# Performance work log

Hardware: AMD Instinct MI355X
Metric: run time of the kernel (lower is better)

Reference implementation:

```python
import jax, jax.numpy as jnp
import numpy as np

B, L, V, D, H, DEPTH, M, FF, NC = 16, 1000, 8, 512, 8, 6, 256, 2048, 1
DH = D // H
SCALE = DH ** -0.5
KCONV = 33  # residual depthwise conv kernel (lucidrains default)


def layer_norm(x, s, b):
    mu = x.mean(-1, keepdims=True)
    var = ((x - mu) ** 2).mean(-1, keepdims=True)
    return (x - mu) * jax.lax.rsqrt(var + 1e-5) * s + b


def moore_penrose_pinv(x, iters=6):
    # iterative Moore-Penrose pseudoinverse (Nystromformer paper / lucidrains)
    I = jnp.eye(x.shape[-1], dtype=x.dtype)
    ax = jnp.abs(x)
    z = jnp.swapaxes(x, -1, -2) / (jnp.max(ax.sum(-1)) * jnp.max(ax.sum(-2)))
    for _ in range(iters):
        xz = x @ z
        z = 0.25 * z @ (13 * I - xz @ (15 * I - xz @ (7 * I - xz)))
    return z


def nystrom_attention(x, qkv_w, out_w, out_b, conv_k):
    b, n, d = x.shape
    pad = (M - n % M) % M  # pad on the LEFT so seq divisible by num_landmarks
    xp = jnp.pad(x, ((0, 0), (pad, 0), (0, 0)))
    N = n + pad
    q, k, v = jnp.split(xp @ qkv_w, 3, axis=-1)
    rh = lambda t: t.reshape(b, N, H, DH).transpose(0, 2, 1, 3)  # bhnd
    q, k, v = rh(q) * SCALE, rh(k), rh(v)
    l = N // M
    q_l = q.reshape(b, H, M, l, DH).mean(3)  # landmark means
    k_l = k.reshape(b, H, M, l, DH).mean(3)
    attn1 = jax.nn.softmax(jnp.einsum('bhnd,bhmd->bhnm', q, k_l), -1)
    attn2 = jax.nn.softmax(jnp.einsum('bhnd,bhmd->bhnm', q_l, k_l), -1)
    attn3 = jax.nn.softmax(jnp.einsum('bhmd,bhnd->bhmn', q_l, k), -1)
    out = (attn1 @ moore_penrose_pinv(attn2)) @ (attn3 @ v)
    # residual depthwise conv over sequence, groups=heads (Conv2d(h,h,(33,1)))
    res = jax.lax.conv_general_dilated(
        v, conv_k, (1, 1), ((KCONV // 2, KCONV // 2), (0, 0)),
        feature_group_count=H, dimension_numbers=('NCHW', 'OIHW', 'NCHW'))
    out = (out + res).transpose(0, 2, 1, 3).reshape(b, N, d)
    out = out @ out_w + out_b
    return out[:, -n:]


def setup_inputs() -> dict:
    key = jax.random.key(0)
    ks = jax.random.split(key, 9)
    s = lambda k, shape, scale=0.02: jax.random.normal(k, shape, jnp.float32) * scale
    return {
        'x': jax.random.randint(ks[0], (B, L), 0, V),
        'enc_emb': s(ks[1], (V, D), 1.0),
        'pos_emb': s(ks[2], (L, D), 1.0),
        'ln1_s': jnp.ones((DEPTH, D)), 'ln1_b': jnp.zeros((DEPTH, D)),
        'qkv_w': s(ks[3], (DEPTH, D, 3 * D)),
        'attn_out_w': s(ks[4], (DEPTH, D, D)), 'attn_out_b': jnp.zeros((DEPTH, D)),
        'conv_k': s(ks[5], (DEPTH, H, 1, KCONV, 1)),
        'ln2_s': jnp.ones((DEPTH, D)), 'ln2_b': jnp.zeros((DEPTH, D)),
        'ff_w1': s(ks[6], (DEPTH, D, FF)), 'ff_b1': jnp.zeros((DEPTH, FF)),
        'ff_w2': s(ks[7], (DEPTH, FF, D)), 'ff_b2': jnp.zeros((DEPTH, D)),
        'final_w': s(ks[8], (D * L, NC)), 'final_b': jnp.zeros((NC,)),
    }


def reference(x, enc_emb, pos_emb, ln1_s, ln1_b, qkv_w, attn_out_w, attn_out_b,
              conv_k, ln2_s, ln2_b, ff_w1, ff_b1, ff_w2, ff_b2, final_w, final_b):
    h = enc_emb[x] + pos_emb[None, :, :]  # token emb + learned posenc
    for i in range(DEPTH):
        h = h + nystrom_attention(layer_norm(h, ln1_s[i], ln1_b[i]),
                                  qkv_w[i], attn_out_w[i], attn_out_b[i], conv_k[i])
        z = layer_norm(h, ln2_s[i], ln2_b[i])
        h = h + jax.nn.gelu(z @ ff_w1[i] + ff_b1[i], approximate=False) @ ff_w2[i] + ff_b2[i]
    out = h.reshape(B, -1) @ final_w + final_b
    return out.reshape(-1)
```

## Files before the change

kernel.cpp:

```cpp
#include <hip/hip_runtime.h>
#include <hip/hip_bf16.h>
#include <math.h>

typedef unsigned short u16;
typedef unsigned int   u32;
typedef __attribute__((ext_vector_type(8))) short short8;
typedef __attribute__((ext_vector_type(4))) float f32x4;

#define L_ 1000
#define D_ 512
#define N_ 1024
#define DEPTH_ 6
#define PAD_ 24
#define SCALE_ 0.125f

__device__ inline float bf2f(u16 u){ union{u32 i; float f;} x; x.i = ((u32)u) << 16; return x.f; }
__device__ inline u16 f2bf(float f){
  union{float f; u32 i;} x; x.f = f;
  u32 r = x.i + 0x7fffu + ((x.i >> 16) & 1u);
  return (u16)(r >> 16);
}

__device__ inline void gld16(const u16* g, u16* l){
  __builtin_amdgcn_global_load_lds(
      (const __attribute__((address_space(1))) unsigned*)g,
      (__attribute__((address_space(3))) unsigned*)l, 16, 0, 0);
}

__device__ inline float blockSum256(float v, float* red){
  int t = threadIdx.x;
  #pragma unroll
  for (int o = 32; o > 0; o >>= 1) v += __shfl_down(v, o, 64);
  __syncthreads();
  if ((t & 63) == 0) red[t >> 6] = v;
  __syncthreads();
  return red[0] + red[1] + red[2] + red[3];
}
__device__ inline float blockMax256(float v, float* red){
  int t = threadIdx.x;
  #pragma unroll
  for (int o = 32; o > 0; o >>= 1) v = fmaxf(v, __shfl_down(v, o, 64));
  __syncthreads();
  if ((t & 63) == 0) red[t >> 6] = v;
  __syncthreads();
  return fmaxf(fmaxf(red[0], red[1]), fmaxf(red[2], red[3]));
}

__global__ __launch_bounds__(256) void embed_kernel(
    const int* __restrict__ x, const float* __restrict__ ee,
    const float* __restrict__ pe, float* __restrict__ h)
{
  long long i = (long long)blockIdx.x * 256 + threadIdx.x;
  int d = (int)(i & 511);
  long long bl = i >> 9;
  int l = (int)(bl % 1000);
  int tok = x[bl];
  h[i] = ee[tok * D_ + d] + pe[l * D_ + d];
}

__global__ __launch_bounds__(256) void ln_kernel(
    const float* __restrict__ in, u16* __restrict__ out,
    const float* __restrict__ sc, const float* __restrict__ bi, int pad)
{
  __shared__ float red[4];
  int r = blockIdx.x, t = threadIdx.x;
  const float* row; u16* orow;
  if (pad){
    int bb = r >> 10, n = r & 1023;
    orow = out + (long long)r * D_;
    if (n < PAD_){ orow[t] = 0; orow[t + 256] = 0; return; }
    row = in + ((long long)bb * L_ + (n - PAD_)) * D_;
  } else {
    row  = in  + (long long)r * D_;
    orow = out + (long long)r * D_;
  }
  float x0 = row[t], x1 = row[t + 256];
  float mu = blockSum256(x0 + x1, red) * (1.f / 512.f);
  float d0 = x0 - mu, d1 = x1 - mu;
  float var = blockSum256(d0 * d0 + d1 * d1, red) * (1.f / 512.f);
  float rs = rsqrtf(var + 1e-5f);
  orow[t]       = f2bf(d0 * rs * sc[t]       + bi[t]);
  orow[t + 256] = f2bf(d1 * rs * sc[t + 256] + bi[t + 256]);
}

__global__ __launch_bounds__(256) void tconv_kernel(
    const float* __restrict__ src, u16* __restrict__ dst, int K, int N)
{
  __shared__ float tile[32][33];
  int kg = blockIdx.y << 5, ng = blockIdx.x << 5;
  int t = threadIdx.x;
  int kr = t >> 3, nc = (t & 7) << 2;
  float4 v = *(const float4*)(src + (long long)(kg + kr) * N + ng + nc);
  tile[kr][nc + 0] = v.x; tile[kr][nc + 1] = v.y;
  tile[kr][nc + 2] = v.z; tile[kr][nc + 3] = v.w;
  __syncthreads();
  int nr = t >> 3, kc = (t & 7) << 2;
  ushort4 o;
  o.x = f2bf(tile[kc + 0][nr]); o.y = f2bf(tile[kc + 1][nr]);
  o.z = f2bf(tile[kc + 2][nr]); o.w = f2bf(tile[kc + 3][nr]);
  *(ushort4*)(dst + (long long)(ng + nr) * K + kg + kc) = o;
}

__global__ __launch_bounds__(256) void vtrans_kernel(
    const u16* __restrict__ qkv, u16* __restrict__ vT)
{
  __shared__ u16 tile[32][36];
  int idx = blockIdx.x;
  int bh = idx >> 6, rem = idx & 63;
  int dt = rem >> 5, nt = rem & 31;
  int b = bh >> 3, hh = bh & 7;
  int t = threadIdx.x;
  {
    int nr = t >> 3, dc = (t & 7) << 2;
    const u16* src = qkv + ((long long)b * N_ + nt * 32 + nr) * 1536 + 1024 + hh * 64 + dt * 32 + dc;
    ushort4 v = *(const ushort4*)src;
    tile[nr][dc + 0] = v.x; tile[nr][dc + 1] = v.y;
    tile[nr][dc + 2] = v.z; tile[nr][dc + 3] = v.w;
  }
  __syncthreads();
  {
    int dr = t >> 3, nc = (t & 7) << 2;
    ushort4 o;
    o.x = tile[nc + 0][dr]; o.y = tile[nc + 1][dr];
    o.z = tile[nc + 2][dr]; o.w = tile[nc + 3][dr];
    *(ushort4*)(vT + (long long)bh * 65536 + (dt * 32 + dr) * 1024 + nt * 32 + nc) = o;
  }
}

template<int OUT, int WC, int TR>
__global__ __launch_bounds__(256) void mgemm(
    const u16* __restrict__ A16, const u16* __restrict__ B16, void* __restrict__ Cv,
    u16* __restrict__ CT, const float* __restrict__ bias,
    int M, int N, int K, int lda, int ldb, int ldc, int ldct,
    long long sAb, long long sAh, long long sBb, long long sBh,
    long long sCb, long long sCh, long long sCT, int nh,
    float scale, float alpha, float beta, int flags)
{
  __shared__ __align__(16) u16 SH[18432];
  u16* As = SH;
  u16* Bs = SH + 8192;

  const int t = threadIdx.x;
  const int bz = blockIdx.z;
  const int b = bz / nh, hh = bz - b * nh;
  const int m0 = blockIdx.y << 7, n0 = blockIdx.x << 7;

  const u16* A = A16 + (long long)b * sAb + (long long)hh * sAh;
  const u16* B = B16 + (long long)b * sBb + (long long)hh * sBh;

  f32x4 acc[4][4];
  #pragma unroll
  for (int i = 0; i < 4; i++)
    #pragma unroll
    for (int j = 0; j < 4; j++) acc[i][j] = (f32x4)0.f;

  const int w = t >> 6, lane = t & 63;
  const int wm = (w >> 1) << 6, wn = (w & 1) << 6;
  const int fr = lane & 15, ko = (lane >> 4) << 3;
  const int sw = (fr & 7) << 3;

  const int sr8 = lane >> 3;
  const int sc8 = ((lane & 7) ^ sr8) << 3;
  const u16* pa[4]; const u16* pb[4]; u16* la[4]; u16* lb[4];
  #pragma unroll
  for (int q = 0; q < 4; q++){
    int ra = min(m0 + w * 32 + q * 8 + sr8, M - 1);
    int rb = min(n0 + w * 32 + q * 8 + sr8, N - 1);
    pa[q] = A + (long long)ra * lda + sc8;
    pb[q] = B + (long long)rb * ldb + sc8;
    la[q] = As + (w * 32 + q * 8) * 64 + lane * 8;
    lb[q] = Bs + (w * 32 + q * 8) * 64 + lane * 8;
  }

  for (int k0 = 0; k0 < K; k0 += 64){
    #pragma unroll
    for (int q = 0; q < 4; q++) gld16(pa[q] + k0, la[q]);
    #pragma unroll
    for (int q = 0; q < 4; q++) gld16(pb[q] + k0, lb[q]);
    __syncthreads();

    #pragma unroll
    for (int ks = 0; ks < 2; ks++){
      short8 ah[4], bhh[4];
      #pragma unroll
      for (int i = 0; i < 4; i++)
        ah[i]  = *(const short8*)(As + (wm + i*16 + fr) * 64 + (((ks << 5) + ko) ^ sw));
      #pragma unroll
      for (int j = 0; j < 4; j++)
        bhh[j] = *(const short8*)(Bs + (wn + j*16 + fr) * 64 + (((ks << 5) + ko) ^ sw));
      #pragma unroll
      for (int i = 0; i < 4; i++)
        #pragma unroll
        for (int j = 0; j < 4; j++)
          acc[i][j] = __builtin_amdgcn_mfma_f32_16x16x32_bf16(ah[i], bhh[j], acc[i][j], 0, 0, 0);
    }
    __syncthreads();
  }

  const long long coff = (long long)b * sCb + (long long)hh * sCh;
  const int quad = (lane >> 4) << 2;
  #pragma unroll
  for (int i = 0; i < 4; i++){
    #pragma unroll
    for (int j = 0; j < 4; j++){
      #pragma unroll
      for (int r = 0; r < 4; r++){
        int row = m0 + wm + i*16 + quad + r;
        int col = n0 + wn + j*16 + fr;
        if (row < M && col < N){
          float v = acc[i][j][r];
          float at = (alpha != 0.f) ? bf2f(A[(long long)row * lda + col]) : 0.f;
          float bt = (beta  != 0.f) ? bf2f(B[(long long)col * ldb + row]) : 0.f;
          v = scale * (alpha * at + beta * bt - v);
          if (flags & 4) v -= (row == col) ? 1.f : 0.f;
          if (bias) v += bias[col];
          if (flags & 2) v = 0.5f * v * (1.f + erff(v * 0.7071067811865476f));
          if constexpr (WC){
            if constexpr (OUT == 0){
              float* cp = (float*)Cv + coff + (long long)row * ldc + col;
              if (flags & 1) v += *cp;
              *cp = v;
            } else {
              u16* cp = (u16*)Cv + coff + (long long)row * ldc + col;
              if (flags & 1) v += bf2f(*cp);
              *cp = f2bf(v);
            }
          }
          if constexpr (TR)
            SH[(wn + j*16 + fr) * 144 + (wm + i*16 + quad + r)] = f2bf(v);
        }
      }
    }
  }
  if constexpr (TR){
    __syncthreads();
    const long long cofft = (long long)bz * sCT;
    #pragma unroll
    for (int c2 = 0; c2 < 8; c2++){
      int idx = c2 * 256 + t;
      int cl = idx >> 4, ms = (idx & 15) << 3;
      int gcol = n0 + cl;
      if (gcol < N && m0 + ms < M){
        uint4 val = *(const uint4*)(SH + cl * 144 + ms);
        *(uint4*)(CT + cofft + (long long)gcol * ldct + m0 + ms) = val;
      }
    }
  }
}

__global__ __launch_bounds__(256) void fattn1_kernel(
    const u16* __restrict__ qkv, const u16* __restrict__ klp,
    const u16* __restrict__ wlT, u16* __restrict__ apre)
{
  __shared__ __align__(16) u16 LDS[20480];
  u16* Qs = LDS;
  u16* Ks = LDS + 4096;
  u16* Ps = LDS;
  const int t = threadIdx.x, w = t >> 6, lane = t & 63;
  const int bh = blockIdx.y, b = bh >> 3, hh = bh & 7;
  const int m0 = blockIdx.x << 6;
  const int fr = lane & 15, ko = (lane >> 4) << 3, sw = (fr & 7) << 3;
  const u16* wl = wlT + (long long)bh * 16384;

  {
    int sr = lane >> 3, sc = ((lane & 7) ^ sr) << 3;
    const u16* qbase = qkv + ((long long)b * N_ + m0) * 1536 + hh * 64 + sc;
    const u16* kbase = klp + (long long)bh * 16384 + sc;
    #pragma unroll
    for (int q = 0; q < 2; q++)
      gld16(qbase + (long long)(w*16 + q*8 + sr) * 1536, Qs + (w*16 + q*8) * 64 + lane * 8);
    #pragma unroll
    for (int q = 0; q < 8; q++)
      gld16(kbase + (w*64 + q*8 + sr) * 64, Ks + (w*64 + q*8) * 64 + lane * 8);
  }
  __syncthreads();

  f32x4 s[16];
  #pragma unroll
  for (int j = 0; j < 16; j++) s[j] = (f32x4)0.f;
  #pragma unroll
  for (int ks = 0; ks < 2; ks++){
    short8 aq = *(const short8*)(Qs + (w*16 + fr) * 64 + (((ks << 5) + ko) ^ sw));
    #pragma unroll
    for (int j = 0; j < 16; j++){
      short8 bk = *(const short8*)(Ks + (j*16 + fr) * 64 + (((ks << 5) + ko) ^ sw));
      s[j] = __builtin_amdgcn_mfma_f32_16x16x32_bf16(aq, bk, s[j], 0, 0, 0);
    }
  }
  __syncthreads();

  const int g4 = (lane >> 4) << 2, c = lane & 15;
  #pragma unroll
  for (int r = 0; r < 4; r++){
    float v[16]; float mx = -3.4e38f;
    #pragma unroll
    for (int j = 0; j < 16; j++){ v[j] = s[j][r] * SCALE_; mx = fmaxf(mx, v[j]); }
    #pragma unroll
    for (int m = 1; m < 16; m <<= 1) mx = fmaxf(mx, __shfl_xor(mx, m, 64));
    float sum = 0.f;
    #pragma unroll
    for (int j = 0; j < 16; j++){ v[j] = expf(v[j] - mx); sum += v[j]; }
    #pragma unroll
    for (int m = 1; m < 16; m <<= 1) sum += __shfl_xor(sum, m, 64);
    float inv = 1.f / sum;
    int row = w*16 + g4 + r;
    #pragma unroll
    for (int j = 0; j < 16; j++) Ps[row * 264 + j*16 + c] = f2bf(v[j] * inv);
  }

  f32x4 o[4];
  #pragma unroll
  for (int j = 0; j < 4; j++) o[j] = (f32x4)0.f;
  #pragma unroll
  for (int ks = 0; ks < 8; ks++){
    short8 ap = *(const short8*)(Ps + (w*16 + fr) * 264 + ks*32 + ko);
    #pragma unroll
    for (int j2 = 0; j2 < 4; j2++){
      short8 bw = *(const short8*)(wl + (j2*16 + fr) * 256 + ks*32 + ko);
      o[j2] = __builtin_amdgcn_mfma_f32_16x16x32_bf16(ap, bw, o[j2], 0, 0, 0);
    }
  }
  u16* ap0 = apre + (long long)b * 524288 + hh * 64;
  #pragma unroll
  for (int j2 = 0; j2 < 4; j2++)
    #pragma unroll
    for (int r = 0; r < 4; r++){
      long long n = m0 + w*16 + g4 + r;
      u16* p = ap0 + n * 512 + j2*16 + c;
      *p = f2bf(bf2f(*p) + o[j2][r]);
    }
}

__global__ __launch_bounds__(256) void fattn2_kernel(
    const u16* __restrict__ ql, const u16* __restrict__ klp, u16* __restrict__ x16)
{
  __shared__ __align__(16) u16 LDS[20480];
  u16* Qs = LDS;
  u16* Ks = LDS + 4096;
  const int t = threadIdx.x, w = t >> 6, lane = t & 63;
  const int bh = blockIdx.y;
  const int m0 = blockIdx.x << 6;
  const int fr = lane & 15, ko = (lane >> 4) << 3, sw = (fr & 7) << 3;

  {
    int sr = lane >> 3, sc = ((lane & 7) ^ sr) << 3;
    const u16* qbase = ql + (long long)bh * 16384 + m0 * 64 + sc;
    const u16* kbase = klp + (long long)bh * 16384 + sc;
    #pragma unroll
    for (int q = 0; q < 2; q++)
      gld16(qbase + (w*16 + q*8 + sr) * 64, Qs + (w*16 + q*8) * 64 + lane * 8);
    #pragma unroll
    for (int q = 0; q < 8; q++)
      gld16(kbase + (w*64 + q*8 + sr) * 64, Ks + (w*64 + q*8) * 64 + lane * 8);
  }
  __syncthreads();

  f32x4 s[16];
  #pragma unroll
  for (int j = 0; j < 16; j++) s[j] = (f32x4)0.f;
  #pragma unroll
  for (int ks = 0; ks < 2; ks++){
    short8 aq = *(const short8*)(Qs + (w*16 + fr) * 64 + (((ks << 5) + ko) ^ sw));
    #pragma unroll
    for (int j = 0; j < 16; j++){
      short8 bk = *(const short8*)(Ks + (j*16 + fr) * 64 + (((ks << 5) + ko) ^ sw));
      s[j] = __builtin_amdgcn_mfma_f32_16x16x32_bf16(aq, bk, s[j], 0, 0, 0);
    }
  }

  const int g4 = (lane >> 4) << 2, c = lane & 15;
  u16* xb = x16 + (long long)bh * 65536;
  #pragma unroll
  for (int r = 0; r < 4; r++){
    float v[16]; float mx = -3.4e38f;
    #pragma unroll
    for (int j = 0; j < 16; j++){ v[j] = s[j][r]; mx = fmaxf(mx, v[j]); }
    #pragma unroll
    for (int m = 1; m < 16; m <<= 1) mx = fmaxf(mx, __shfl_xor(mx, m, 64));
    float sum = 0.f;
    #pragma unroll
    for (int j = 0; j < 16; j++){ v[j] = expf(v[j] - mx); sum += v[j]; }
    #pragma unroll
    for (int m = 1; m < 16; m <<= 1) sum += __shfl_xor(sum, m, 64);
    float inv = 1.f / sum;
    int row = m0 + w*16 + g4 + r;
    #pragma unroll
    for (int j = 0; j < 16; j++) xb[(long long)row * 256 + j*16 + c] = f2bf(v[j] * inv);
  }
}

template<int PER>
__global__ __launch_bounds__(256) void softmax_bf16(u16* __restrict__ d)
{
  __shared__ float red[4];
  long long r = blockIdx.x;
  u16* row = d + r * (PER * 256);
  int t = threadIdx.x;
  float vals[PER];
  float mx = -3.4e38f;
  #pragma unroll
  for (int i = 0; i < PER; i++){ vals[i] = bf2f(row[t + i * 256]); mx = fmaxf(mx, vals[i]); }
  mx = blockMax256(mx, red);
  float s = 0.f;
  #pragma unroll
  for (int i = 0; i < PER; i++){ vals[i] = expf(vals[i] - mx); s += vals[i]; }
  s = blockSum256(s, red);
  float inv = 1.f / s;
  #pragma unroll
  for (int i = 0; i < PER; i++) row[t + i * 256] = f2bf(vals[i] * inv);
}

__global__ __launch_bounds__(256) void landmark_kernel(
    const u16* __restrict__ qkv, u16* __restrict__ ql, u16* __restrict__ kl)
{
  long long i = (long long)blockIdx.x * 256 + threadIdx.x;
  int d = (int)(i & 63);
  long long r = i >> 6;
  int m = (int)(r & 255);
  int bh = (int)(r >> 8);
  int hh = bh & 7, b = bh >> 3;
  const u16* base = qkv + ((long long)b * N_ + m * 4) * 1536 + hh * 64 + d;
  float qs = bf2f(base[0]) + bf2f(base[1536]) + bf2f(base[3072]) + bf2f(base[4608]);
  float ks = bf2f(base[512]) + bf2f(base[2048]) + bf2f(base[3584]) + bf2f(base[5120]);
  ql[i] = f2bf(qs * 0.25f * SCALE_);
  kl[i] = f2bf(ks * 0.25f);
}

__global__ void zero_kernel(float* p, int n){
  int i = blockIdx.x * 64 + threadIdx.x;
  if (i < n) p[i] = 0.f;
}
__global__ __launch_bounds__(256) void rcmax_kernel(
    const u16* __restrict__ x, float* __restrict__ scal)
{
  __shared__ float red[4];
  int bid = blockIdx.x, t = threadIdx.x;
  if (bid < 128){
    const u16* X = x + (long long)bid * 65536;
    float cs = 0.f;
    for (int m = 0; m < 256; m++) cs += fabsf(bf2f(X[m * 256 + t]));
    float cmax = blockMax256(cs, red);
    if (t == 0) atomicMax((unsigned int*)(scal + 1), __float_as_uint(cmax));
  } else {
    const u16* X = x + (long long)(bid - 128) * 65536;
    float rs = 0.f;
    for (int j = 0; j < 256; j++) rs += fabsf(bf2f(X[t * 256 + j]));
    float rmax = blockMax256(rs, red);
    if (t == 0) atomicMax((unsigned int*)(scal + 0), __float_as_uint(rmax));
  }
}
__global__ __launch_bounds__(256) void zinit_kernel(
    const u16* __restrict__ x, u16* __restrict__ z, u16* __restrict__ zt,
    const float* __restrict__ scal)
{
  float inv = 1.f / (scal[0] * scal[1]);
  long long i = (long long)blockIdx.x * 256 + threadIdx.x;
  long long bh = i >> 16;
  int ij = (int)(i & 65535);
  int ii = ij >> 8, jj = ij & 255;
  z[i]  = f2bf(bf2f(x[(bh << 16) + (jj << 8) + ii]) * inv);
  zt[i] = f2bf(bf2f(x[i]) * inv);
}

__global__ __launch_bounds__(256) void conv_kernel(
    const u16* __restrict__ qkv, const float* __restrict__ ck, u16* __restrict__ out)
{
  __shared__ u16 V[40 * 512];
  int idx = blockIdx.x;
  int b = idx >> 7, n0 = (idx & 127) << 3;
  int t = threadIdx.x;
  #pragma unroll
  for (int i = 0; i < 10; i++){
    int s = t + i * 256;
    int row = s >> 6, col8 = (s & 63) << 3;
    int n = n0 - 16 + row;
    uint4 v = make_uint4(0,0,0,0);
    if (n >= 0 && n < N_)
      v = *(const uint4*)(qkv + ((long long)b * N_ + n) * 1536 + 1024 + col8);
    *(uint4*)(V + row * 512 + col8) = v;
  }
  __syncthreads();
  int hh = t >> 5;
  float wts[33];
  #pragma unroll
  for (int k = 0; k < 33; k++) wts[k] = ck[hh * 33 + k];
  const u32* Vw = (const u32*)V;
  u32* O = (u32*)out;
  #pragma unroll 2
  for (int nn = 0; nn < 8; nn++){
    float a0 = 0.f, a1 = 0.f;
    #pragma unroll
    for (int k = 0; k < 33; k++){
      u32 pv = Vw[(nn + k) * 256 + t];
      a0 += bf2f((u16)(pv & 0xffffu)) * wts[k];
      a1 += bf2f((u16)(pv >> 16))     * wts[k];
    }
    O[((long long)b * N_ + n0 + nn) * 256 + t] = (u32)f2bf(a0) | ((u32)f2bf(a1) << 16);
  }
}

__global__ __launch_bounds__(256) void final_kernel(
    const float* __restrict__ h, const float* __restrict__ w,
    const float* __restrict__ bb, float* __restrict__ out)
{
  __shared__ float red[4];
  int b = blockIdx.x, t = threadIdx.x;
  const float* hp = h + (long long)b * (L_ * D_);
  float acc = 0.f;
  for (int i = t; i < L_ * D_; i += 256) acc += hp[i] * w[i];
  acc = blockSum256(acc, red);
  if (t == 0) out[b] = acc + bb[0];
}

template<int OUT, int WC, int TR>
static inline void mg(hipStream_t st, const void* A, const void* B, void* C, void* CT,
  const float* bias, int M, int N, int K, int lda, int ldb, int ldc, int ldct,
  long long sAb, long long sAh, long long sBb, long long sBh,
  long long sCb, long long sCh, long long sCT, int batch, int nh,
  float scale, float alpha, float beta, int flags)
{
  dim3 g((N + 127) >> 7, (M + 127) >> 7, batch);
  mgemm<OUT, WC, TR><<<g, 256, 0, st>>>((const u16*)A, (const u16*)B, C, (u16*)CT, bias,
      M, N, K, lda, ldb, ldc, ldct, sAb, sAh, sBb, sBh, sCb, sCh, sCT, nh,
      scale, alpha, beta, flags);
}

extern "C" void kernel_launch(void* const* d_in, const int* in_sizes, int n_in,
                              void* d_out, int out_size, void* d_ws, size_t ws_size,
                              hipStream_t stream)
{
  const int*   xin  = (const int*)d_in[0];
  const float* enc  = (const float*)d_in[1];
  const float* pos  = (const float*)d_in[2];
  const float* ln1s = (const float*)d_in[3];
  const float* ln1b = (const float*)d_in[4];
  const float* qkvw = (const float*)d_in[5];
  const float* ow   = (const float*)d_in[6];
  const float* ob   = (const float*)d_in[7];
  const float* ck   = (const float*)d_in[8];
  const float* ln2s = (const float*)d_in[9];
  const float* ln2b = (const float*)d_in[10];
  const float* w1   = (const float*)d_in[11];
  const float* b1   = (const float*)d_in[12];
  const float* w2   = (const float*)d_in[13];
  const float* b2   = (const float*)d_in[14];
  const float* fw   = (const float*)d_in[15];
  const float* fb   = (const float*)d_in[16];
  float* out = (float*)d_out;

  const size_t NEED = 223608896ULL;
  if (ws_size < NEED) return;

  const long long SL = 16777216;
  char* P = (char*)d_ws;
  float* h    = (float*)P; P += 32768000;
  u16*   X16  = (u16*)P;   P += 16777216;
  char*  R    = P;         P += 6 * SL;
  u16*   qkv  = (u16*)P;   P += 50331648;
  u16*   ql   = (u16*)P;   P += 4194304;
  u16*   kl   = (u16*)P;   P += 4194304;
  u16*   a3vT = (u16*)P;   P += 4194304;
  u16*   WlT  = (u16*)P;   P += 4194304;
  u16*   qkvwT= (u16*)P;   P += 1572864;
  u16*   owT  = (u16*)P;   P += 524288;
  u16*   w1T  = (u16*)P;   P += 2097152;
  u16*   w2T  = (u16*)P;   P += 2097152;
  float* scal = (float*)P; P += 64;

  u16* probs3 = (u16*)R;
  u16* vT     = (u16*)(R + 4*SL);
  u16* Em     = (u16*)(R + 0*SL);
  u16* ET     = (u16*)(R + 1*SL);
  u16* Za     = (u16*)(R + 2*SL);
  u16* Zb     = (u16*)(R + 3*SL);
  u16* T1     = (u16*)(R + 4*SL);
  u16* T2     = (u16*)(R + 5*SL);
  u16* probs1 = (u16*)R;
  u16* apre   = (u16*)(R + 4*SL);
  u16* xln    = (u16*)(R + 5*SL);

  embed_kernel<<<32000, 256, 0, stream>>>(xin, enc, pos, h);

  for (int i = 0; i < DEPTH_; i++){
    tconv_kernel<<<dim3(48, 16), 256, 0, stream>>>(qkvw + (long long)i * 786432, qkvwT, 512, 1536);
    tconv_kernel<<<dim3(16, 16), 256, 0, stream>>>(ow + (long long)i * 262144, owT, 512, 512);
    tconv_kernel<<<dim3(64, 16), 256, 0, stream>>>(w1 + (long long)i * 1048576, w1T, 512, 2048);
    tconv_kernel<<<dim3(16, 64), 256, 0, stream>>>(w2 + (long long)i * 1048576, w2T, 2048, 512);

    ln_kernel<<<16384, 256, 0, stream>>>(h, xln, ln1s + i * 512, ln1b + i * 512, 1);

    mg<1,1,0>(stream, xln, qkvwT, qkv, nullptr, nullptr, 16384, 1536, 512, 512, 512, 1536, 0,
              0,0, 0,0, 0,0, 0, 1, 1, -1.f, 0.f, 0.f, 0);

    landmark_kernel<<<8192, 256, 0, stream>>>(qkv, ql, kl);
    vtrans_kernel<<<8192, 256, 0, stream>>>(qkv, vT);

    fattn2_kernel<<<dim3(4, 128), 256, 0, stream>>>(ql, kl, X16);

    mg<1,1,0>(stream, ql, qkv + 512, probs3, nullptr, nullptr, 256, 1024, 64, 64, 1536, 1024, 0,
              131072, 16384, 1572864, 64, 2097152, 262144, 0, 128, 8, -1.f, 0.f, 0.f, 0);
    softmax_bf16<4><<<32768, 256, 0, stream>>>(probs3);
    mg<1,0,1>(stream, probs3, vT, nullptr, a3vT, nullptr, 256, 64, 1024, 1024, 1024, 0, 256,
              2097152, 262144, 524288, 65536, 0, 0, 16384, 128, 8, -1.f, 0.f, 0.f, 0);

    zero_kernel<<<1, 64, 0, stream>>>(scal, 16);
    rcmax_kernel<<<256, 256, 0, stream>>>(X16, scal);

    zinit_kernel<<<32768, 256, 0, stream>>>(X16, Za, T1, scal);
    mg<1,1,1>(stream, X16, T1, Em, ET, nullptr, 256, 256, 256, 256, 256, 256, 256,
              65536, 0, 65536, 0, 65536, 0, 65536, 128, 1, -1.f, 0.f, 0.f, 4);
    u16 *Zc = Za, *Zn = Zb;
    for (int it = 0; it < 6; it++){
      mg<1,0,1>(stream, Em, ET, nullptr, T1, nullptr, 256, 256, 256, 256, 256, 0, 256,
                65536, 0, 65536, 0, 0, 0, 65536, 128, 1, 1.f, 5.f, 0.f, 0);
      mg<1,0,1>(stream, Em, T1, nullptr, T2, nullptr, 256, 256, 256, 256, 256, 0, 256,
                65536, 0, 65536, 0, 0, 0, 65536, 128, 1, 1.f, 9.f, -1.f, 0);
      mg<1,1,1>(stream, Zc, T2, Zn, T1, nullptr, 256, 256, 256, 256, 256, 256, 256,
                65536, 0, 65536, 0, 65536, 0, 65536, 128, 1, 0.25f, 4.f, 0.f, 0);
      if (it < 5)
        mg<1,1,1>(stream, X16, T1, Em, ET, nullptr, 256, 256, 256, 256, 256, 256, 256,
                  65536, 0, 65536, 0, 65536, 0, 65536, 128, 1, -1.f, 0.f, 0.f, 4);
      u16* tmp = Zc; Zc = Zn; Zn = tmp;
    }
    mg<1,0,1>(stream, Zc, a3vT, nullptr, WlT, nullptr, 256, 64, 256, 256, 256, 0, 256,
              65536, 0, 16384, 0, 0, 0, 16384, 128, 1, -1.f, 0.f, 0.f, 0);

    conv_kernel<<<2048, 256, 0, stream>>>(qkv, ck + i * 264, apre);

    fattn1_kernel<<<dim3(16, 128), 256, 0, stream>>>(qkv, kl, WlT, apre);

    mg<0,1,0>(stream, apre + PAD_ * 512, owT, h, nullptr, ob + i * 512,
              1000, 512, 512, 512, 512, 512, 0,
              524288, 0, 0, 0, 512000, 0, 0, 16, 1, -1.f, 0.f, 0.f, 1);

    ln_kernel<<<16000, 256, 0, stream>>>(h, xln, ln2s + i * 512, ln2b + i * 512, 0);

    for (int c = 0; c < 2; c++){
      mg<1,1,0>(stream, xln, w1T + (long long)c * 1024 * 512, probs1, nullptr,
                b1 + i * 2048 + c * 1024, 16000, 1024, 512, 512, 512, 1024, 0,
                0,0, 0,0, 0,0, 0, 1, 1, -1.f, 0.f, 0.f, 2);
      mg<0,1,0>(stream, probs1, w2T + (long long)c * 1024, h, nullptr,
                (c == 0) ? (b2 + i * 512) : nullptr,
                16000, 512, 1024, 1024, 2048, 512, 0,
                0,0, 0,0, 0,0, 0, 1, 1, -1.f, 0.f, 0.f, 1);
    }
  }

  final_kernel<<<16, 256, 0, stream>>>(h, fw, fb, out);
}
```

Measured before the change: 9.080 ms.

## Fuse Newton-Schulz pinv loop, attn3 flash softmax, and weight transposes into single kernels

```diff
diff --git a/kernel.cpp b/kernel.cpp
--- a/kernel.cpp
+++ b/kernel.cpp
@@ -83,11 +83,20 @@
   orow[t + 256] = f2bf(d1 * rs * sc[t + 256] + bi[t + 256]);
 }
 
-__global__ __launch_bounds__(256) void tconv_kernel(
-    const float* __restrict__ src, u16* __restrict__ dst, int K, int N)
+__global__ __launch_bounds__(256) void tconv4_kernel(
+    const float* __restrict__ qkvw, const float* __restrict__ ow,
+    const float* __restrict__ w1, const float* __restrict__ w2,
+    u16* __restrict__ qkvwT, u16* __restrict__ owT,
+    u16* __restrict__ w1T, u16* __restrict__ w2T, int layer)
 {
   __shared__ float tile[32][33];
-  int kg = blockIdx.y << 5, ng = blockIdx.x << 5;
+  int id = blockIdx.x;
+  const float* src; u16* dst; int K, N, bx, by;
+  if (id < 768)      { src = qkvw + (long long)layer * 786432;  dst = qkvwT; K = 512;  N = 1536; bx = id % 48; by = id / 48; }
+  else if (id < 1024){ id -= 768;  src = ow + (long long)layer * 262144;  dst = owT; K = 512;  N = 512;  bx = id % 16; by = id / 16; }
+  else if (id < 2048){ id -= 1024; src = w1 + (long long)layer * 1048576; dst = w1T; K = 512;  N = 2048; bx = id % 64; by = id / 64; }
+  else               { id -= 2048; src = w2 + (long long)layer * 1048576; dst = w2T; K = 2048; N = 512;  bx = id % 16; by = id / 16; }
+  int kg = by << 5, ng = bx << 5;
   int t = threadIdx.x;
   int kr = t >> 3, nc = (t & 7) << 2;
   float4 v = *(const float4*)(src + (long long)(kg + kr) * N + ng + nc);
@@ -248,6 +257,205 @@
   }
 }
 
+#define TBX(c, r) ((c) * 72 + (((((r) >> 3)) ^ ((c) & 7)) << 3) + ((r) & 7))
+
+template<int WC, int WT, int ID, int NC>
+__device__ inline void gstep(const u16* __restrict__ A, const u16* __restrict__ B,
+                             u16* C, u16* CT, float scale, float alpha, float beta,
+                             int w, int lane, u16* tb)
+{
+  const int wr = w >> 2, wc = w & 3;
+  if (NC == 64 && wc != 0) return;
+  const int wm = wr << 6, wn = wc << 6;
+  const int fr = lane & 15, ko = (lane >> 4) << 3, quad = (lane >> 4) << 2;
+  f32x4 acc[4][4];
+  #pragma unroll
+  for (int i = 0; i < 4; i++)
+    #pragma unroll
+    for (int j = 0; j < 4; j++) acc[i][j] = (f32x4)0.f;
+  #pragma unroll
+  for (int k0 = 0; k0 < 256; k0 += 32){
+    short8 a4[4], b4[4];
+    #pragma unroll
+    for (int i = 0; i < 4; i++) a4[i] = *(const short8*)(A + (wm + i*16 + fr) * 256 + k0 + ko);
+    #pragma unroll
+    for (int j = 0; j < 4; j++) b4[j] = *(const short8*)(B + (wn + j*16 + fr) * 256 + k0 + ko);
+    #pragma unroll
+    for (int i = 0; i < 4; i++)
+      #pragma unroll
+      for (int j = 0; j < 4; j++)
+        acc[i][j] = __builtin_amdgcn_mfma_f32_16x16x32_bf16(a4[i], b4[j], acc[i][j], 0, 0, 0);
+  }
+  #pragma unroll
+  for (int i = 0; i < 4; i++)
+    #pragma unroll
+    for (int j = 0; j < 4; j++)
+      #pragma unroll
+      for (int r = 0; r < 4; r++){
+        int row = wm + i*16 + quad + r, col = wn + j*16 + fr;
+        float v = acc[i][j][r];
+        float at = (alpha != 0.f) ? bf2f(A[row * 256 + col]) : 0.f;
+        float bt = (beta  != 0.f) ? bf2f(B[col * 256 + row]) : 0.f;
+        v = scale * (alpha * at + beta * bt - v);
+        if (ID) v -= (row == col) ? 1.f : 0.f;
+        u16 bv = f2bf(v);
+        if (WC) C[row * 256 + col] = bv;
+        if (WT) tb[TBX(col - wn, row - wm)] = bv;
+      }
+  if (WT){
+    #pragma unroll
+    for (int p = 0; p < 8; p++){
+      short8 xv = *(const short8*)(tb + lane * 72 + (p << 3));
+      int lq = p ^ (lane & 7);
+      *(short8*)(CT + (long long)(wn + lane) * 256 + wm + (lq << 3)) = xv;
+    }
+  }
+}
+
+__global__ __launch_bounds__(1024) void ns_kernel(
+    const u16* __restrict__ X, const u16* __restrict__ a3vT,
+    u16* __restrict__ Za, u16* __restrict__ Zb,
+    u16* __restrict__ Em, u16* __restrict__ ET,
+    u16* __restrict__ T1, u16* __restrict__ T2,
+    u16* __restrict__ WlT, const float* __restrict__ scal)
+{
+  __shared__ __align__(16) u16 TBUF[16][4608];
+  const int t = threadIdx.x, w = t >> 6, lane = t & 63;
+  const long long off = (long long)blockIdx.x << 16;
+  const u16* Xb  = X + off;
+  const u16* a3b = a3vT + ((long long)blockIdx.x << 14);
+  u16 *Zab = Za + off, *Zbb = Zb + off, *Emb = Em + off, *ETb = ET + off;
+  u16 *T1b = T1 + off, *T2b = T2 + off, *Wb = WlT + ((long long)blockIdx.x << 14);
+  const float inv = 1.f / (scal[0] * scal[1]);
+  u16* tb = &TBUF[w][0];
+  const int wr = w >> 2, wc = w & 3;
+  const int wm = wr << 6, wn = wc << 6;
+
+  {
+    #pragma unroll
+    for (int it = 0; it < 8; it++){
+      int r = (lane >> 3) + it * 8;
+      int c0 = (lane & 7) << 3;
+      short8 xv = *(const short8*)(Xb + (long long)(wm + r) * 256 + wn + c0);
+      #pragma unroll
+      for (int e = 0; e < 8; e++)
+        tb[TBX(c0 + e, r)] = f2bf(bf2f(((const u16*)&xv)[e]) * inv);
+    }
+    #pragma unroll
+    for (int p = 0; p < 8; p++){
+      short8 xv = *(const short8*)(tb + lane * 72 + (p << 3));
+      int lq = p ^ (lane & 7);
+      *(short8*)(Zab + (long long)(wn + lane) * 256 + wm + (lq << 3)) = xv;
+    }
+  }
+  __syncthreads();
+
+  gstep<1,1,1,256>(Xb, Xb, Emb, ETb, -inv, 0.f, 0.f, w, lane, tb);
+  __syncthreads();
+
+  u16 *Zc = Zab, *Zn = Zbb;
+  for (int it = 0; it < 6; it++){
+    gstep<0,1,0,256>(Emb, ETb, nullptr, T1b, 1.f, 5.f, 0.f, w, lane, tb);
+    __syncthreads();
+    gstep<0,1,0,256>(Emb, T1b, nullptr, T2b, 1.f, 9.f, -1.f, w, lane, tb);
+    __syncthreads();
+    gstep<1,1,0,256>(Zc, T2b, Zn, T1b, 0.25f, 4.f, 0.f, w, lane, tb);
+    __syncthreads();
+    if (it < 5){
+      gstep<1,1,1,256>(Xb, T1b, Emb, ETb, -1.f, 0.f, 0.f, w, lane, tb);
+      __syncthreads();
+    }
+    u16* tmp = Zc; Zc = Zn; Zn = tmp;
+  }
+  gstep<0,1,0,64>(Zc, a3b, nullptr, Wb, -1.f, 0.f, 0.f, w, lane, tb);
+}
+
+__global__ __launch_bounds__(256) void fattn3_kernel(
+    const u16* __restrict__ ql, const u16* __restrict__ qkv,
+    const u16* __restrict__ vT, u16* __restrict__ a3vT)
+{
+  __shared__ __align__(16) u16 Ps[4][4224];
+  __shared__ __align__(16) u16 TB[4][1280];
+  const int t = threadIdx.x, w = t >> 6, lane = t & 63;
+  const int bh = blockIdx.y, b = bh >> 3, hh = bh & 7;
+  const int m0 = blockIdx.x << 6;
+  const int fr = lane & 15, ko = (lane >> 4) << 3, quad = (lane >> 4) << 2;
+  const u16* qb = ql + ((long long)bh << 14) + (m0 + w * 16) * 64;
+  const u16* kb = qkv + (long long)b * (N_ * 1536) + 512 + hh * 64;
+  const u16* vb = vT + ((long long)bh << 16);
+  u16* ps = &Ps[w][0];
+
+  short8 aq[2];
+  aq[0] = *(const short8*)(qb + fr * 64 + ko);
+  aq[1] = *(const short8*)(qb + fr * 64 + 32 + ko);
+
+  f32x4 o[4];
+  #pragma unroll
+  for (int j = 0; j < 4; j++) o[j] = (f32x4)0.f;
+  float mrow[4] = {-1e38f, -1e38f, -1e38f, -1e38f};
+  float lrow[4] = {0.f, 0.f, 0.f, 0.f};
+
+  for (int kt = 0; kt < 4; kt++){
+    f32x4 s[16];
+    #pragma unroll
+    for (int j = 0; j < 16; j++) s[j] = (f32x4)0.f;
+    #pragma unroll
+    for (int ks = 0; ks < 2; ks++)
+      #pragma unroll
+      for (int j = 0; j < 16; j++){
+        short8 bk = *(const short8*)(kb + (long long)(kt * 256 + j * 16 + fr) * 1536 + ks * 32 + ko);
+        s[j] = __builtin_amdgcn_mfma_f32_16x16x32_bf16(aq[ks], bk, s[j], 0, 0, 0);
+      }
+    float corr[4];
+    #pragma unroll
+    for (int r = 0; r < 4; r++){
+      float mx = s[0][r];
+      #pragma unroll
+      for (int j = 1; j < 16; j++) mx = fmaxf(mx, s[j][r]);
+      #pragma unroll
+      for (int mk = 1; mk < 16; mk <<= 1) mx = fmaxf(mx, __shfl_xor(mx, mk, 64));
+      float nm = fmaxf(mrow[r], mx);
+      corr[r] = expf(mrow[r] - nm);
+      mrow[r] = nm;
+      float psum = 0.f;
+      #pragma unroll
+      for (int j = 0; j < 16; j++){
+        float p = expf(s[j][r] - nm);
+        psum += p;
+        ps[(quad + r) * 264 + j * 16 + fr] = f2bf(p);
+      }
+      #pragma unroll
+      for (int mk = 1; mk < 16; mk <<= 1) psum += __shfl_xor(psum, mk, 64);
+      lrow[r] = lrow[r] * corr[r] + psum;
+    }
+    #pragma unroll
+    for (int j = 0; j < 4; j++)
+      #pragma unroll
+      for (int r = 0; r < 4; r++) o[j][r] *= corr[r];
+    #pragma unroll
+    for (int ks = 0; ks < 8; ks++){
+      short8 ap = *(const short8*)(ps + fr * 264 + ks * 32 + ko);
+      #pragma unroll
+      for (int j2 = 0; j2 < 4; j2++){
+        short8 bv = *(const short8*)(vb + (j2 * 16 + fr) * 1024 + kt * 256 + ks * 32 + ko);
+        o[j2] = __builtin_amdgcn_mfma_f32_16x16x32_bf16(ap, bv, o[j2], 0, 0, 0);
+      }
+    }
+  }
+  u16* tbw = &TB[w][0];
+  #pragma unroll
+  for (int j2 = 0; j2 < 4; j2++)
+    #pragma unroll
+    for (int r = 0; r < 4; r++)
+      tbw[(j2 * 16 + fr) * 20 + quad + r] = f2bf(o[j2][r] / lrow[r]);
+  u16* ob = a3vT + ((long long)bh << 14) + m0 + w * 16;
+  #pragma unroll
+  for (int q4 = 0; q4 < 4; q4++){
+    ushort4 xv = *(const ushort4*)(tbw + lane * 20 + q4 * 4);
+    *(ushort4*)(ob + (long long)lane * 256 + q4 * 4) = xv;
+  }
+}
+
 __global__ __launch_bounds__(256) void fattn1_kernel(
     const u16* __restrict__ qkv, const u16* __restrict__ klp,
     const u16* __restrict__ wlT, u16* __restrict__ apre)
@@ -387,27 +595,6 @@
     #pragma unroll
     for (int j = 0; j < 16; j++) xb[(long long)row * 256 + j*16 + c] = f2bf(v[j] * inv);
   }
-}
-
-template<int PER>
-__global__ __launch_bounds__(256) void softmax_bf16(u16* __restrict__ d)
-{
-  __shared__ float red[4];
-  long long r = blockIdx.x;
-  u16* row = d + r * (PER * 256);
-  int t = threadIdx.x;
-  float vals[PER];
-  float mx = -3.4e38f;
-  #pragma unroll
-  for (int i = 0; i < PER; i++){ vals[i] = bf2f(row[t + i * 256]); mx = fmaxf(mx, vals[i]); }
-  mx = blockMax256(mx, red);
-  float s = 0.f;
-  #pragma unroll
-  for (int i = 0; i < PER; i++){ vals[i] = expf(vals[i] - mx); s += vals[i]; }
-  s = blockSum256(s, red);
-  float inv = 1.f / s;
-  #pragma unroll
-  for (int i = 0; i < PER; i++) row[t + i * 256] = f2bf(vals[i] * inv);
 }
 
 __global__ __launch_bounds__(256) void landmark_kernel(
@@ -448,18 +635,6 @@
     float rmax = blockMax256(rs, red);
     if (t == 0) atomicMax((unsigned int*)(scal + 0), __float_as_uint(rmax));
   }
-}
-__global__ __launch_bounds__(256) void zinit_kernel(
-    const u16* __restrict__ x, u16* __restrict__ z, u16* __restrict__ zt,
-    const float* __restrict__ scal)
-{
-  float inv = 1.f / (scal[0] * scal[1]);
-  long long i = (long long)blockIdx.x * 256 + threadIdx.x;
-  long long bh = i >> 16;
-  int ij = (int)(i & 65535);
-  int ii = ij >> 8, jj = ij & 255;
-  z[i]  = f2bf(bf2f(x[(bh << 16) + (jj << 8) + ii]) * inv);
-  zt[i] = f2bf(bf2f(x[i]) * inv);
 }
 
 __global__ __launch_bounds__(256) void conv_kernel(
@@ -567,7 +742,6 @@
   u16*   w2T  = (u16*)P;   P += 2097152;
   float* scal = (float*)P; P += 64;
 
-  u16* probs3 = (u16*)R;
   u16* vT     = (u16*)(R + 4*SL);
   u16* Em     = (u16*)(R + 0*SL);
   u16* ET     = (u16*)(R + 1*SL);
@@ -582,10 +756,7 @@
   embed_kernel<<<32000, 256, 0, stream>>>(xin, enc, pos, h);
 
   for (int i = 0; i < DEPTH_; i++){
-    tconv_kernel<<<dim3(48, 16), 256, 0, stream>>>(qkvw + (long long)i * 786432, qkvwT, 512, 1536);
-    tconv_kernel<<<dim3(16, 16), 256, 0, stream>>>(ow + (long long)i * 262144, owT, 512, 512);
-    tconv_kernel<<<dim3(64, 16), 256, 0, stream>>>(w1 + (long long)i * 1048576, w1T, 512, 2048);
-    tconv_kernel<<<dim3(16, 64), 256, 0, stream>>>(w2 + (long long)i * 1048576, w2T, 2048, 512);
+    tconv4_kernel<<<3072, 256, 0, stream>>>(qkvw, ow, w1, w2, qkvwT, owT, w1T, w2T, i);
 
     ln_kernel<<<16384, 256, 0, stream>>>(h, xln, ln1s + i * 512, ln1b + i * 512, 1);
 
@@ -597,33 +768,12 @@
 
     fattn2_kernel<<<dim3(4, 128), 256, 0, stream>>>(ql, kl, X16);
 
-    mg<1,1,0>(stream, ql, qkv + 512, probs3, nullptr, nullptr, 256, 1024, 64, 64, 1536, 1024, 0,
-              131072, 16384, 1572864, 64, 2097152, 262144, 0, 128, 8, -1.f, 0.f, 0.f, 0);
-    softmax_bf16<4><<<32768, 256, 0, stream>>>(probs3);
-    mg<1,0,1>(stream, probs3, vT, nullptr, a3vT, nullptr, 256, 64, 1024, 1024, 1024, 0, 256,
-              2097152, 262144, 524288, 65536, 0, 0, 16384, 128, 8, -1.f, 0.f, 0.f, 0);
+    fattn3_kernel<<<dim3(4, 128), 256, 0, stream>>>(ql, qkv, vT, a3vT);
 
     zero_kernel<<<1, 64, 0, stream>>>(scal, 16);
     rcmax_kernel<<<256, 256, 0, stream>>>(X16, scal);
 
-    zinit_kernel<<<32768, 256, 0, stream>>>(X16, Za, T1, scal);
-    mg<1,1,1>(stream, X16, T1, Em, ET, nullptr, 256, 256, 256, 256, 256, 256, 256,
-              65536, 0, 65536, 0, 65536, 0, 65536, 128, 1, -1.f, 0.f, 0.f, 4);
-    u16 *Zc = Za, *Zn = Zb;
-    for (int it = 0; it < 6; it++){
-      mg<1,0,1>(stream, Em, ET, nullptr, T1, nullptr, 256, 256, 256, 256, 256, 0, 256,
-                65536, 0, 65536, 0, 0, 0, 65536, 128, 1, 1.f, 5.f, 0.f, 0);
-      mg<1,0,1>(stream, Em, T1, nullptr, T2, nullptr, 256, 256, 256, 256, 256, 0, 256,
-                65536, 0, 65536, 0, 0, 0, 65536, 128, 1, 1.f, 9.f, -1.f, 0);
-      mg<1,1,1>(stream, Zc, T2, Zn, T1, nullptr, 256, 256, 256, 256, 256, 256, 256,
-                65536, 0, 65536, 0, 65536, 0, 65536, 128, 1, 0.25f, 4.f, 0.f, 0);
-      if (it < 5)
-        mg<1,1,1>(stream, X16, T1, Em, ET, nullptr, 256, 256, 256, 256, 256, 256, 256,
-                  65536, 0, 65536, 0, 65536, 0, 65536, 128, 1, -1.f, 0.f, 0.f, 4);
-      u16* tmp = Zc; Zc = Zn; Zn = tmp;
-    }
-    mg<1,0,1>(stream, Zc, a3vT, nullptr, WlT, nullptr, 256, 64, 256, 256, 256, 0, 256,
-              65536, 0, 16384, 0, 0, 0, 16384, 128, 1, -1.f, 0.f, 0.f, 0);
+    ns_kernel<<<128, 1024, 0, stream>>>(X16, a3vT, Za, Zb, Em, ET, T1, T2, WlT, scal);
 
     conv_kernel<<<2048, 256, 0, stream>>>(qkv, ck + i * 264, apre);
 
```

New measurement: 14.27 ms. 1.57x slower.

## Fuse landmark-query attention into flash-style kernel and merge weight transposes

Applied to the files above, without the earlier changes.

```diff
diff --git a/kernel.cpp b/kernel.cpp
--- a/kernel.cpp
+++ b/kernel.cpp
@@ -83,11 +83,20 @@
   orow[t + 256] = f2bf(d1 * rs * sc[t + 256] + bi[t + 256]);
 }
 
-__global__ __launch_bounds__(256) void tconv_kernel(
-    const float* __restrict__ src, u16* __restrict__ dst, int K, int N)
+__global__ __launch_bounds__(256) void tconv4_kernel(
+    const float* __restrict__ qkvw, const float* __restrict__ ow,
+    const float* __restrict__ w1, const float* __restrict__ w2,
+    u16* __restrict__ qkvwT, u16* __restrict__ owT,
+    u16* __restrict__ w1T, u16* __restrict__ w2T, int layer)
 {
   __shared__ float tile[32][33];
-  int kg = blockIdx.y << 5, ng = blockIdx.x << 5;
+  int id = blockIdx.x;
+  const float* src; u16* dst; int K, N, bx, by;
+  if (id < 768)      { src = qkvw + (long long)layer * 786432;  dst = qkvwT; K = 512;  N = 1536; bx = id % 48; by = id / 48; }
+  else if (id < 1024){ id -= 768;  src = ow + (long long)layer * 262144;  dst = owT; K = 512;  N = 512;  bx = id % 16; by = id / 16; }
+  else if (id < 2048){ id -= 1024; src = w1 + (long long)layer * 1048576; dst = w1T; K = 512;  N = 2048; bx = id % 64; by = id / 64; }
+  else               { id -= 2048; src = w2 + (long long)layer * 1048576; dst = w2T; K = 2048; N = 512;  bx = id % 16; by = id / 16; }
+  int kg = by << 5, ng = bx << 5;
   int t = threadIdx.x;
   int kr = t >> 3, nc = (t & 7) << 2;
   float4 v = *(const float4*)(src + (long long)(kg + kr) * N + ng + nc);
@@ -248,6 +257,92 @@
   }
 }
 
+__global__ __launch_bounds__(256) void fattn3_kernel(
+    const u16* __restrict__ ql, const u16* __restrict__ qkv,
+    const u16* __restrict__ vT, u16* __restrict__ a3vT)
+{
+  __shared__ __align__(16) u16 Ps[4][4224];
+  __shared__ __align__(16) u16 TB[4][1280];
+  const int t = threadIdx.x, w = t >> 6, lane = t & 63;
+  const int bh = blockIdx.y, b = bh >> 3, hh = bh & 7;
+  const int m0 = blockIdx.x << 6;
+  const int fr = lane & 15, ko = (lane >> 4) << 3, quad = (lane >> 4) << 2;
+  const u16* qb = ql + ((long long)bh << 14) + (m0 + w * 16) * 64;
+  const u16* kb = qkv + (long long)b * (N_ * 1536) + 512 + hh * 64;
+  const u16* vb = vT + ((long long)bh << 16);
+  u16* ps = &Ps[w][0];
+
+  short8 aq[2];
+  aq[0] = *(const short8*)(qb + fr * 64 + ko);
+  aq[1] = *(const short8*)(qb + fr * 64 + 32 + ko);
+
+  f32x4 o[4];
+  #pragma unroll
+  for (int j = 0; j < 4; j++) o[j] = (f32x4)0.f;
+  float mrow[4] = {-1e38f, -1e38f, -1e38f, -1e38f};
+  float lrow[4] = {0.f, 0.f, 0.f, 0.f};
+
+  for (int kt = 0; kt < 4; kt++){
+    f32x4 s[16];
+    #pragma unroll
+    for (int j = 0; j < 16; j++) s[j] = (f32x4)0.f;
+    #pragma unroll
+    for (int ks = 0; ks < 2; ks++)
+      #pragma unroll
+      for (int j = 0; j < 16; j++){
+        short8 bk = *(const short8*)(kb + (long long)(kt * 256 + j * 16 + fr) * 1536 + ks * 32 + ko);
+        s[j] = __builtin_amdgcn_mfma_f32_16x16x32_bf16(aq[ks], bk, s[j], 0, 0, 0);
+      }
+    float corr[4];
+    #pragma unroll
+    for (int r = 0; r < 4; r++){
+      float mx = s[0][r];
+      #pragma unroll
+      for (int j = 1; j < 16; j++) mx = fmaxf(mx, s[j][r]);
+      #pragma unroll
+      for (int mk = 1; mk < 16; mk <<= 1) mx = fmaxf(mx, __shfl_xor(mx, mk, 64));
+      float nm = fmaxf(mrow[r], mx);
+      corr[r] = expf(mrow[r] - nm);
+      mrow[r] = nm;
+      float psum = 0.f;
+      #pragma unroll
+      for (int j = 0; j < 16; j++){
+        float p = expf(s[j][r] - nm);
+        psum += p;
+        ps[(quad + r) * 264 + j * 16 + fr] = f2bf(p);
+      }
+      #pragma unroll
+      for (int mk = 1; mk < 16; mk <<= 1) psum += __shfl_xor(psum, mk, 64);
+      lrow[r] = lrow[r] * corr[r] + psum;
+    }
+    #pragma unroll
+    for (int j = 0; j < 4; j++)
+      #pragma unroll
+      for (int r = 0; r < 4; r++) o[j][r] *= corr[r];
+    #pragma unroll
+    for (int ks = 0; ks < 8; ks++){
+      short8 ap = *(const short8*)(ps + fr * 264 + ks * 32 + ko);
+      #pragma unroll
+      for (int j2 = 0; j2 < 4; j2++){
+        short8 bv = *(const short8*)(vb + (j2 * 16 + fr) * 1024 + kt * 256 + ks * 32 + ko);
+        o[j2] = __builtin_amdgcn_mfma_f32_16x16x32_bf16(ap, bv, o[j2], 0, 0, 0);
+      }
+    }
+  }
+  u16* tbw = &TB[w][0];
+  #pragma unroll
+  for (int j2 = 0; j2 < 4; j2++)
+    #pragma unroll
+    for (int r = 0; r < 4; r++)
+      tbw[(j2 * 16 + fr) * 20 + quad + r] = f2bf(o[j2][r] / lrow[r]);
+  u16* ob = a3vT + ((long long)bh << 14) + m0 + w * 16;
+  #pragma unroll
+  for (int q4 = 0; q4 < 4; q4++){
+    ushort4 xv = *(const ushort4*)(tbw + lane * 20 + q4 * 4);
+    *(ushort4*)(ob + (long long)lane * 256 + q4 * 4) = xv;
+  }
+}
+
 __global__ __launch_bounds__(256) void fattn1_kernel(
     const u16* __restrict__ qkv, const u16* __restrict__ klp,
     const u16* __restrict__ wlT, u16* __restrict__ apre)
@@ -387,27 +482,6 @@
     #pragma unroll
     for (int j = 0; j < 16; j++) xb[(long long)row * 256 + j*16 + c] = f2bf(v[j] * inv);
   }
-}
-
-template<int PER>
-__global__ __launch_bounds__(256) void softmax_bf16(u16* __restrict__ d)
-{
-  __shared__ float red[4];
-  long long r = blockIdx.x;
-  u16* row = d + r * (PER * 256);
-  int t = threadIdx.x;
-  float vals[PER];
-  float mx = -3.4e38f;
-  #pragma unroll
-  for (int i = 0; i < PER; i++){ vals[i] = bf2f(row[t + i * 256]); mx = fmaxf(mx, vals[i]); }
-  mx = blockMax256(mx, red);
-  float s = 0.f;
-  #pragma unroll
-  for (int i = 0; i < PER; i++){ vals[i] = expf(vals[i] - mx); s += vals[i]; }
-  s = blockSum256(s, red);
-  float inv = 1.f / s;
-  #pragma unroll
-  for (int i = 0; i < PER; i++) row[t + i * 256] = f2bf(vals[i] * inv);
 }
 
 __global__ __launch_bounds__(256) void landmark_kernel(
@@ -567,7 +641,6 @@
   u16*   w2T  = (u16*)P;   P += 2097152;
   float* scal = (float*)P; P += 64;
 
-  u16* probs3 = (u16*)R;
   u16* vT     = (u16*)(R + 4*SL);
   u16* Em     = (u16*)(R + 0*SL);
   u16* ET     = (u16*)(R + 1*SL);
@@ -582,10 +655,7 @@
   embed_kernel<<<32000, 256, 0, stream>>>(xin, enc, pos, h);
 
   for (int i = 0; i < DEPTH_; i++){
-    tconv_kernel<<<dim3(48, 16), 256, 0, stream>>>(qkvw + (long long)i * 786432, qkvwT, 512, 1536);
-    tconv_kernel<<<dim3(16, 16), 256, 0, stream>>>(ow + (long long)i * 262144, owT, 512, 512);
-    tconv_kernel<<<dim3(64, 16), 256, 0, stream>>>(w1 + (long long)i * 1048576, w1T, 512, 2048);
-    tconv_kernel<<<dim3(16, 64), 256, 0, stream>>>(w2 + (long long)i * 1048576, w2T, 2048, 512);
+    tconv4_kernel<<<3072, 256, 0, stream>>>(qkvw, ow, w1, w2, qkvwT, owT, w1T, w2T, i);
 
     ln_kernel<<<16384, 256, 0, stream>>>(h, xln, ln1s + i * 512, ln1b + i * 512, 1);
 
@@ -597,11 +667,7 @@
 
     fattn2_kernel<<<dim3(4, 128), 256, 0, stream>>>(ql, kl, X16);
 
-    mg<1,1,0>(stream, ql, qkv + 512, probs3, nullptr, nullptr, 256, 1024, 64, 64, 1536, 1024, 0,
-              131072, 16384, 1572864, 64, 2097152, 262144, 0, 128, 8, -1.f, 0.f, 0.f, 0);
-    softmax_bf16<4><<<32768, 256, 0, stream>>>(probs3);
-    mg<1,0,1>(stream, probs3, vT, nullptr, a3vT, nullptr, 256, 64, 1024, 1024, 1024, 0, 256,
-              2097152, 262144, 524288, 65536, 0, 0, 16384, 128, 8, -1.f, 0.f, 0.f, 0);
+    fattn3_kernel<<<dim3(4, 128), 256, 0, stream>>>(ql, qkv, vT, a3vT);
 
     zero_kernel<<<1, 64, 0, stream>>>(scal, 16);
     rcmax_kernel<<<256, 256, 0, stream>>>(X16, scal);
```

Result: no change. 9.010 ms (-0.8%).
